# Optimization experiments

Hardware: AMD Instinct MI355X
Metric: run time of the kernel (lower is better)

## Reference

```python
import jax, jax.numpy as jnp
import numpy as np

N, E, G = 50000, 640000, 2000
F_NODE, F_EDGE, H, L, T = 64, 16, 128, 2, 2


def _seg_softmax(logits, idx, num_seg):
    # logits: [E], idx: [E] -> softmax per segment
    m = jax.ops.segment_max(logits, idx, num_segments=num_seg)
    e = jnp.exp(logits - m[idx])
    s = jax.ops.segment_sum(e, idx, num_segments=num_seg)
    return e / (s[idx] + 1e-16)


def _gru(x, h, Wih, Whh, bih, bhh):
    gi = x @ Wih + bih
    gh = h @ Whh + bhh
    ir, iz, inn = jnp.split(gi, 3, axis=-1)
    hr, hz, hn = jnp.split(gh, 3, axis=-1)
    r = jax.nn.sigmoid(ir + hr)
    z = jax.nn.sigmoid(iz + hz)
    n = jnp.tanh(inn + r * hn)
    return (1.0 - z) * n + z * h


def setup_inputs() -> dict:
    key = jax.random.key(0)
    ks = jax.random.split(key, 30)
    s = 0.05
    inp = {
        'x': jax.random.normal(ks[0], (N, F_NODE), jnp.float32),
        'edge_index': jax.random.randint(ks[1], (2, E), 0, N, jnp.int32),
        'edge_attr': jax.random.normal(ks[2], (E, F_EDGE), jnp.float32),
        'batch': jnp.sort(jax.random.randint(ks[3], (N,), 0, G, jnp.int32)),
        'emb_W': jax.random.normal(ks[4], (F_NODE, H), jnp.float32) * s,
        'emb_b': jnp.zeros((H,), jnp.float32),
        'attW1': jax.random.normal(ks[5], (L, 2 * H + F_EDGE, H), jnp.float32) * s,
        'attb1': jnp.zeros((L, H), jnp.float32),
        'attW2': jax.random.normal(ks[6], (L, H, 1), jnp.float32) * s,
        'attb2': jnp.zeros((L, 1), jnp.float32),
        'mlpW': jax.random.normal(ks[7], (L, H + F_EDGE, H), jnp.float32) * s,
        'mlpb': jnp.zeros((L, H), jnp.float32),
        'gru_Wih': jax.random.normal(ks[8], (L, H, 3 * H), jnp.float32) * s,
        'gru_Whh': jax.random.normal(ks[9], (L, H, 3 * H), jnp.float32) * s,
        'gru_bih': jnp.zeros((L, 3 * H), jnp.float32),
        'gru_bhh': jnp.zeros((L, 3 * H), jnp.float32),
        'gattW1': jax.random.normal(ks[10], (H, H), jnp.float32) * s,
        'gattb1': jnp.zeros((H,), jnp.float32),
        'gattW2': jax.random.normal(ks[11], (H, 1), jnp.float32) * s,
        'gattb2': jnp.zeros((1,), jnp.float32),
        'ggru_Wih': jax.random.normal(ks[12], (H, 3 * H), jnp.float32) * s,
        'ggru_Whh': jax.random.normal(ks[13], (H, 3 * H), jnp.float32) * s,
        'ggru_bih': jnp.zeros((3 * H,), jnp.float32),
        'ggru_bhh': jnp.zeros((3 * H,), jnp.float32),
    }
    return inp


def reference(x, edge_index, edge_attr, batch, emb_W, emb_b, attW1, attb1,
              attW2, attb2, mlpW, mlpb, gru_Wih, gru_Whh, gru_bih, gru_bhh,
              gattW1, gattb1, gattW2, gattb2, ggru_Wih, ggru_Whh, ggru_bih,
              ggru_bhh):
    src, dst = edge_index[0], edge_index[1]  # PyG: x_j = x[src], x_i = x[dst]
    h = jax.nn.relu(x @ emb_W + emb_b)  # [N, H]
    for l in range(L):
        x_i, x_j = h[dst], h[src]                       # [E, H] gathers
        cat = jnp.concatenate([x_i, x_j, edge_attr], axis=-1)  # [E, 2H+F_e]
        a = jax.nn.leaky_relu(cat @ attW1[l] + attb1[l], 0.2) @ attW2[l] + attb2[l]
        alpha = _seg_softmax(a[:, 0], dst, N)[:, None]  # segment softmax over dst
        msg = jax.nn.relu(jnp.concatenate([x_j, edge_attr], axis=-1) @ mlpW[l] + mlpb[l])
        aggr = jax.ops.segment_sum(alpha * msg, dst, num_segments=N)  # [N, H]
        h = _gru(aggr, h, gru_Wih[l], gru_Whh[l], gru_bih[l], gru_bhh[l])
    g = jax.ops.segment_sum(h, batch, num_segments=G)  # global_add_pool [G, H]
    for _ in range(T):
        s = jnp.tanh(h @ gattW1 + gattb1) @ gattW2 + gattb2  # [N, 1]
        att = _seg_softmax(s[:, 0], batch, G)[:, None]
        ctx = jax.ops.segment_sum(att * h, batch, num_segments=G)
        g = _gru(ctx, g, ggru_Wih, ggru_Whh, ggru_bih, ggru_bhh)
    return g
```

## Files before the change

### kernel.cpp

```cpp
#include <hip/hip_runtime.h>
#include <hip/hip_bf16.h>
#include <math.h>

#define N_NODES 50000
#define N_EDGES 640000
#define N_GRAPHS 2000
#define FN 64
#define FE 16
#define H 128
#define NL 2
#define DPW 4
#define SCB 1024

typedef __attribute__((ext_vector_type(8))) short short8;
typedef __attribute__((ext_vector_type(4))) float float4v;
typedef __hip_bfloat16 bf16;

static constexpr size_t AL = 256;
static constexpr size_t alup(size_t x) { return (x + AL - 1) & ~(AL - 1); }

static constexpr size_t SZ_HF    = (size_t)N_NODES * H * 4;
static constexpr size_t SZ_HB    = (size_t)N_NODES * H * 2;
static constexpr size_t SZ_XB    = (size_t)N_NODES * FN * 2;
static constexpr size_t SZ_PQMB  = (size_t)N_NODES * 384 * 2;
static constexpr size_t SZ_GH    = (size_t)N_NODES * 384 * 4;
static constexpr size_t SZ_GI    = (size_t)N_NODES * 384 * 4;
static constexpr size_t SZ_AGB   = (size_t)N_NODES * H * 2;
static constexpr size_t SZ_NF    = (size_t)N_NODES * 4;
static constexpr size_t SZ_WT    = (size_t)768 * 128 * 2;
static constexpr size_t SZ_WIHT  = (size_t)384 * 128 * 2;
static constexpr size_t SZ_EMBT  = (size_t)128 * 64 * 2;
static constexpr size_t SZ_BBIG  = (size_t)768 * 4;
static constexpr size_t SZ_G128  = (size_t)N_GRAPHS * 128 * 4;
static constexpr size_t SZ_G384  = (size_t)N_GRAPHS * 384 * 4;
static constexpr size_t SZ_GF    = (size_t)N_GRAPHS * 4;
static constexpr size_t SZ_CSE   = (size_t)N_EDGES * 8;
static constexpr size_t SZ_BSUM  = 256 * 4;

static constexpr size_t OFF_H0    = 0;
static constexpr size_t OFF_H1    = alup(OFF_H0 + SZ_HF);
static constexpr size_t OFF_H0B   = alup(OFF_H1 + SZ_HF);
static constexpr size_t OFF_H1B   = alup(OFF_H0B + SZ_HB);
static constexpr size_t OFF_XB    = alup(OFF_H1B + SZ_HB);
static constexpr size_t OFF_PQMB  = alup(OFF_XB + SZ_XB);
static constexpr size_t OFF_GH    = alup(OFF_PQMB + SZ_PQMB);
static constexpr size_t OFF_GI    = alup(OFF_GH + SZ_GH);
static constexpr size_t OFF_AGB   = alup(OFF_GI + SZ_GI);
static constexpr size_t OFF_ES    = alup(OFF_AGB + SZ_AGB);
static constexpr size_t OFF_WT    = alup(OFF_ES + SZ_NF);
static constexpr size_t OFF_WIHT  = alup(OFF_WT + SZ_WT);
static constexpr size_t OFF_EMBT  = alup(OFF_WIHT + SZ_WIHT);
static constexpr size_t OFF_BBIG  = alup(OFF_EMBT + SZ_EMBT);
static constexpr size_t OFF_G0    = alup(OFF_BBIG + SZ_BBIG);
static constexpr size_t OFF_GA    = alup(OFF_G0 + SZ_G128);
static constexpr size_t OFF_CTX   = alup(OFF_GA + SZ_G128);
static constexpr size_t OFF_GICTX = alup(OFF_CTX + SZ_G128);
static constexpr size_t OFF_GHB   = alup(OFF_GICTX + SZ_G384);
static constexpr size_t OFF_GSUM  = alup(OFF_GHB + SZ_G384);
static constexpr size_t OFF_DEG   = alup(OFF_GSUM + SZ_GF);
static constexpr size_t OFF_OFFS  = alup(OFF_DEG + SZ_NF);
static constexpr size_t OFF_CUR   = alup(OFF_OFFS + SZ_NF + 4);
static constexpr size_t OFF_CSE   = alup(OFF_CUR + SZ_NF);
static constexpr size_t OFF_GHIST = alup(OFF_CSE + SZ_CSE);
static constexpr size_t OFF_GOFFS = alup(OFF_GHIST + SZ_GF);
static constexpr size_t OFF_BSUM  = alup(OFF_GOFFS + SZ_GF + 4);
static constexpr size_t TOTAL_WS  = alup(OFF_BSUM + SZ_BSUM);

__device__ unsigned char g_afp_ws[TOTAL_WS];

__device__ inline float bf2f(unsigned short u) {
    unsigned int x = ((unsigned int)u) << 16;
    return __uint_as_float(x);
}

template<int K>
__global__ __launch_bounds__(256) void gemm_mfma(
    const bf16* __restrict__ Abf, const bf16* __restrict__ Btbf,
    const float* __restrict__ bias, float* __restrict__ C,
    bf16* __restrict__ Cb, bf16* __restrict__ Cb2,
    int M, int Ncol, int mode)
{
    const unsigned short* A  = (const unsigned short*)Abf;
    const unsigned short* Bt = (const unsigned short*)Btbf;
    const int l  = threadIdx.x & 63;
    const int w  = threadIdx.x >> 6;
    const int wm = w >> 1, wn = w & 1;
    const int row0 = blockIdx.x * 64 + wm * 32;
    const int col0 = blockIdx.y * 64 + wn * 32;
    const int lr = l & 15;
    const int lk = (l >> 4) * 8;
    float4v acc[2][2] = {};
    #pragma unroll
    for (int k0 = 0; k0 < K; k0 += 32) {
        short8 a[2], b[2];
        #pragma unroll
        for (int i = 0; i < 2; ++i) {
            int r = row0 + i * 16 + lr;
            if (r >= M) r = M - 1;
            a[i] = *(const short8*)(A + (size_t)r * K + k0 + lk);
        }
        #pragma unroll
        for (int j = 0; j < 2; ++j) {
            int c = col0 + j * 16 + lr;
            b[j] = *(const short8*)(Bt + (size_t)c * K + k0 + lk);
        }
        #pragma unroll
        for (int i = 0; i < 2; ++i)
            #pragma unroll
            for (int j = 0; j < 2; ++j)
                acc[i][j] = __builtin_amdgcn_mfma_f32_16x16x32_bf16(a[i], b[j], acc[i][j], 0, 0, 0);
    }
    const int orow = (l >> 4) * 4;
    const int ocol = l & 15;
    #pragma unroll
    for (int i = 0; i < 2; ++i) {
        #pragma unroll
        for (int j = 0; j < 2; ++j) {
            const int gc = col0 + j * 16 + ocol;
            const float bi = bias ? bias[gc] : 0.f;
            #pragma unroll
            for (int r = 0; r < 4; ++r) {
                const int gr = row0 + i * 16 + orow + r;
                if (gr >= M) continue;
                float v = acc[i][j][r] + bi;
                if (mode & 1) v = fmaxf(v, 0.f);
                if (mode & 2) {
                    if (gc < 384) Cb[(size_t)gr * 384 + gc] = __float2bfloat16(v);
                    else          Cb2[(size_t)gr * 384 + (gc - 384)] = __float2bfloat16(v);
                } else {
                    C[(size_t)gr * Ncol + gc] = v;
                    if (mode & 4) Cb[(size_t)gr * Ncol + gc] = __float2bfloat16(v);
                }
            }
        }
    }
}

__global__ __launch_bounds__(256) void gemm_gru(
    const bf16* __restrict__ Abf, const bf16* __restrict__ Btbf,
    const float* __restrict__ bias, const bf16* __restrict__ ghb,
    const float* __restrict__ hold, float* __restrict__ hnew,
    bf16* __restrict__ hnewb, int M)
{
    const unsigned short* A  = (const unsigned short*)Abf;
    const unsigned short* Bt = (const unsigned short*)Btbf;
    const unsigned short* gh = (const unsigned short*)ghb;
    const int l  = threadIdx.x & 63;
    const int w  = threadIdx.x >> 6;
    const int row0 = blockIdx.x * 64 + w * 16;
    const int lr = l & 15;
    const int lk = (l >> 4) * 8;
    float4v acc[24] = {};
    #pragma unroll
    for (int k0 = 0; k0 < 128; k0 += 32) {
        int r = row0 + lr;
        if (r >= M) r = M - 1;
        short8 a = *(const short8*)(A + (size_t)r * 128 + k0 + lk);
        #pragma unroll
        for (int j = 0; j < 24; ++j) {
            short8 b = *(const short8*)(Bt + (size_t)(j * 16 + lr) * 128 + k0 + lk);
            acc[j] = __builtin_amdgcn_mfma_f32_16x16x32_bf16(a, b, acc[j], 0, 0, 0);
        }
    }
    const int orow = (l >> 4) * 4;
    const int ocol = l & 15;
    #pragma unroll
    for (int a_ = 0; a_ < 8; ++a_) {
        const int c = a_ * 16 + ocol;
        const float bir = bias[c], biz = bias[c + 128], bin = bias[c + 256];
        #pragma unroll
        for (int r = 0; r < 4; ++r) {
            const int gr = row0 + orow + r;
            if (gr >= M) continue;
            float ir = acc[a_][r] + bir;
            float iz = acc[a_ + 8][r] + biz;
            float in = acc[a_ + 16][r] + bin;
            const unsigned short* ghp = gh + (size_t)gr * 384;
            float hr = bf2f(ghp[c]);
            float hz = bf2f(ghp[128 + c]);
            float hn = bf2f(ghp[256 + c]);
            float rg = 1.f / (1.f + __expf(-(ir + hr)));
            float zg = 1.f / (1.f + __expf(-(iz + hz)));
            float ng = tanhf(in + rg * hn);
            float hv = hold[(size_t)gr * 128 + c];
            float o = (1.f - zg) * ng + zg * hv;
            hnew[(size_t)gr * 128 + c] = o;
            hnewb[(size_t)gr * 128 + c] = __float2bfloat16(o);
        }
    }
}

#define GBM 64
#define GBN 64
#define GBK 32
__global__ __launch_bounds__(256) void gemm_f32(
    const float* __restrict__ A, const float* __restrict__ B,
    const float* __restrict__ bias, float* __restrict__ C,
    int M, int K, int Ncol)
{
    __shared__ float As[GBK][GBM + 4];
    __shared__ float Bs[GBK][GBN + 4];
    const int tx = threadIdx.x & 15;
    const int ty = threadIdx.x >> 4;
    const int row0 = blockIdx.x * GBM;
    const int col0 = blockIdx.y * GBN;
    float acc[4][4] = {};
    for (int k0 = 0; k0 < K; k0 += GBK) {
        for (int i = threadIdx.x; i < GBM * GBK; i += 256) {
            int r = i / GBK, c = i % GBK;
            float v = 0.f;
            if (row0 + r < M) v = A[(size_t)(row0 + r) * K + k0 + c];
            As[c][r] = v;
        }
        for (int i = threadIdx.x; i < GBK * GBN; i += 256) {
            int r = i / GBN, c = i % GBN;
            float v = 0.f;
            if (col0 + c < Ncol) v = B[(size_t)(k0 + r) * Ncol + col0 + c];
            Bs[r][c] = v;
        }
        __syncthreads();
        #pragma unroll
        for (int k = 0; k < GBK; ++k) {
            float a[4], b[4];
            #pragma unroll
            for (int i = 0; i < 4; ++i) a[i] = As[k][ty * 4 + i];
            #pragma unroll
            for (int j = 0; j < 4; ++j) b[j] = Bs[k][tx * 4 + j];
            #pragma unroll
            for (int i = 0; i < 4; ++i)
                #pragma unroll
                for (int j = 0; j < 4; ++j)
                    acc[i][j] = fmaf(a[i], b[j], acc[i][j]);
        }
        __syncthreads();
    }
    #pragma unroll
    for (int i = 0; i < 4; ++i) {
        int r = row0 + ty * 4 + i;
        if (r >= M) continue;
        #pragma unroll
        for (int j = 0; j < 4; ++j) {
            int c = col0 + tx * 4 + j;
            if (c >= Ncol) continue;
            C[(size_t)r * Ncol + c] = acc[i][j] + (bias ? bias[c] : 0.f);
        }
    }
}

__global__ void pack_weights_bt(const float* __restrict__ attW1,
                                const float* __restrict__ mlpW,
                                const float* __restrict__ whh,
                                const float* __restrict__ attb1,
                                const float* __restrict__ mlpb,
                                const float* __restrict__ bhh,
                                bf16* __restrict__ wt, float* __restrict__ bbig)
{
    int idx = blockIdx.x * blockDim.x + threadIdx.x;
    if (idx >= 768 * 128) return;
    int j = idx >> 7, k = idx & 127;
    float v;
    if (j < 128)      v = attW1[k * 128 + j];
    else if (j < 256) v = attW1[(128 + k) * 128 + (j - 128)];
    else if (j < 384) v = mlpW[k * 128 + (j - 256)];
    else              v = whh[k * 384 + (j - 384)];
    wt[idx] = __float2bfloat16(v);
    if (k == 0) {
        float b;
        if (j < 128)      b = attb1[j];
        else if (j < 256) b = 0.f;
        else if (j < 384) b = mlpb[j - 256];
        else              b = bhh[j - 384];
        bbig[j] = b;
    }
}

__global__ void transpose_cast(const float* __restrict__ in, bf16* __restrict__ out,
                               int K, int Ncol)
{
    int idx = blockIdx.x * blockDim.x + threadIdx.x;
    if (idx >= K * Ncol) return;
    int k = idx / Ncol, j = idx % Ncol;
    out[(size_t)j * K + k] = __float2bfloat16(in[idx]);
}

__global__ void cast_bf16_kernel(const float* __restrict__ in, bf16* __restrict__ out, int n)
{
    int idx = blockIdx.x * blockDim.x + threadIdx.x;
    if (idx < n) out[idx] = __float2bfloat16(in[idx]);
}

__global__ void hist_dst_kernel(const int* __restrict__ ei, int* __restrict__ deg) {
    int e = blockIdx.x * blockDim.x + threadIdx.x;
    if (e < N_EDGES) atomicAdd(&deg[ei[N_EDGES + e]], 1);
}
__global__ void hist_batch_kernel(const int* __restrict__ batch, int* __restrict__ hist) {
    int n = blockIdx.x * blockDim.x + threadIdx.x;
    if (n < N_NODES) atomicAdd(&hist[batch[n]], 1);
}

__global__ __launch_bounds__(1024) void scan_local(const int* __restrict__ in,
        int* __restrict__ out, int* __restrict__ bsum, int n)
{
    __shared__ int buf[SCB];
    int i = blockIdx.x * SCB + threadIdx.x;
    int v = (i < n) ? in[i] : 0;
    buf[threadIdx.x] = v;
    __syncthreads();
    #pragma unroll
    for (int off = 1; off < SCB; off <<= 1) {
        int t = (threadIdx.x >= off) ? buf[threadIdx.x - off] : 0;
        __syncthreads();
        buf[threadIdx.x] += t;
        __syncthreads();
    }
    if (i < n) out[i] = buf[threadIdx.x] - v;
    if (threadIdx.x == SCB - 1) bsum[blockIdx.x] = buf[SCB - 1];
}
__global__ __launch_bounds__(1024) void scan_bsum(int* __restrict__ bsum, int nb,
        int* __restrict__ total_dst)
{
    __shared__ int buf[SCB];
    int v = (threadIdx.x < nb) ? bsum[threadIdx.x] : 0;
    buf[threadIdx.x] = v;
    __syncthreads();
    #pragma unroll
    for (int off = 1; off < SCB; off <<= 1) {
        int t = (threadIdx.x >= off) ? buf[threadIdx.x - off] : 0;
        __syncthreads();
        buf[threadIdx.x] += t;
        __syncthreads();
    }
    if (threadIdx.x < nb) bsum[threadIdx.x] = buf[threadIdx.x] - v;
    if (threadIdx.x == 0) *total_dst = buf[SCB - 1];
}
__global__ __launch_bounds__(1024) void scan_addoff(int* __restrict__ out,
        const int* __restrict__ bsum, int n)
{
    int i = blockIdx.x * SCB + threadIdx.x;
    if (i < n) out[i] += bsum[blockIdx.x];
}

__global__ void scatter_cse_kernel(const int* __restrict__ ei, const int* __restrict__ offs,
                                   int* __restrict__ cur, int2* __restrict__ cse) {
    int e = blockIdx.x * blockDim.x + threadIdx.x;
    if (e >= N_EDGES) return;
    int d = ei[N_EDGES + e];
    int pos = offs[d] + atomicAdd(&cur[d], 1);
    cse[pos] = make_int2(ei[e], e);
}

__global__ __launch_bounds__(256, 2) void edge_fused_kernel(
    const bf16* __restrict__ pqm_b,
    const int2* __restrict__ cse, const float* __restrict__ ea,
    const float* __restrict__ w1c_g, const float* __restrict__ w2_g,
    const float* __restrict__ b2_g, const float* __restrict__ mlpw2_g,
    const int* __restrict__ offs, bf16* __restrict__ aggrb)
{
    const unsigned short* pqm = (const unsigned short*)pqm_b;
    const int wv = threadIdx.x >> 6, lane = threadIdx.x & 63;
    const int c0 = lane * 2;
    float w1r[16][2], wmr[16][2];
    #pragma unroll
    for (int k = 0; k < 16; ++k) {
        w1r[k][0] = w1c_g[k * 128 + c0];
        w1r[k][1] = w1c_g[k * 128 + c0 + 1];
        wmr[k][0] = mlpw2_g[k * 128 + c0];
        wmr[k][1] = mlpw2_g[k * 128 + c0 + 1];
    }
    const float w20 = w2_g[c0], w21 = w2_g[c0 + 1];
    const float b2 = b2_g[0];
    const int dbase = __builtin_amdgcn_readfirstlane((blockIdx.x * 4 + wv) * DPW);

    for (int rep = 0; rep < DPW; ++rep) {
        const int d = dbase + rep;
        if (d >= N_NODES) break;
        const ushort2 pu = *(const ushort2*)(pqm + (size_t)d * 384 + c0);
        const float p0 = bf2f(pu.x), p1 = bf2f(pu.y);
        float acc0 = 0.f, acc1 = 0.f, ssum = 0.f;
        const int b = offs[d], en = offs[d + 1];
        if (b < en) {
            int2 se = cse[b];
            const unsigned short* ps = pqm + (size_t)se.x * 384;
            ushort2 qu = *(const ushort2*)(ps + 128 + c0);
            ushort2 mu = *(const ushort2*)(ps + 256 + c0);
            const float4* eap = (const float4*)(ea + (size_t)se.y * 16);
            float4 e0 = eap[0], e1 = eap[1], e2 = eap[2], e3 = eap[3];
            float sp_p = 0.f, m0_p = 0.f, m1_p = 0.f, gate = 0.f;
            for (int i = b; i < en; ++i) {
                float t0 = p0 + bf2f(qu.x), t1 = p1 + bf2f(qu.y);
                float m0 = bf2f(mu.x), m1 = bf2f(mu.y);
                float er[16];
                er[0]=e0.x; er[1]=e0.y; er[2]=e0.z; er[3]=e0.w;
                er[4]=e1.x; er[5]=e1.y; er[6]=e1.z; er[7]=e1.w;
                er[8]=e2.x; er[9]=e2.y; er[10]=e2.z; er[11]=e2.w;
                er[12]=e3.x; er[13]=e3.y; er[14]=e3.z; er[15]=e3.w;
                if (i + 1 < en) {
                    se = cse[i + 1];
                    const unsigned short* psn = pqm + (size_t)se.x * 384;
                    qu = *(const ushort2*)(psn + 128 + c0);
                    mu = *(const ushort2*)(psn + 256 + c0);
                    const float4* eapn = (const float4*)(ea + (size_t)se.y * 16);
                    e0 = eapn[0]; e1 = eapn[1]; e2 = eapn[2]; e3 = eapn[3];
                }
                float sps = sp_p;
                #pragma unroll
                for (int off = 32; off; off >>= 1) sps += __shfl_xor(sps, off);
                const float ex = gate * __expf(sps + b2);
                ssum += ex;
                acc0 = fmaf(ex, fmaxf(m0_p, 0.f), acc0);
                acc1 = fmaf(ex, fmaxf(m1_p, 0.f), acc1);
                #pragma unroll
                for (int k = 0; k < 16; ++k) {
                    t0 = fmaf(er[k], w1r[k][0], t0);
                    t1 = fmaf(er[k], w1r[k][1], t1);
                    m0 = fmaf(er[k], wmr[k][0], m0);
                    m1 = fmaf(er[k], wmr[k][1], m1);
                }
                float a0 = (t0 > 0.f) ? t0 : 0.2f * t0;
                float a1 = (t1 > 0.f) ? t1 : 0.2f * t1;
                sp_p = a0 * w20 + a1 * w21;
                m0_p = m0; m1_p = m1;
                gate = 1.f;
            }
            float sps = sp_p;
            #pragma unroll
            for (int off = 32; off; off >>= 1) sps += __shfl_xor(sps, off);
            const float ex = __expf(sps + b2);
            ssum += ex;
            acc0 = fmaf(ex, fmaxf(m0_p, 0.f), acc0);
            acc1 = fmaf(ex, fmaxf(m1_p, 0.f), acc1);
        }
        const float inv = 1.f / (ssum + 1e-16f);
        bf16* outp = aggrb + (size_t)d * 128 + c0;
        outp[0] = __float2bfloat16(acc0 * inv);
        outp[1] = __float2bfloat16(acc1 * inv);
    }
}

__global__ void gru_elem_kernel(const float* __restrict__ gi,
                                const float* __restrict__ gh,
                                const float* __restrict__ hold, float* __restrict__ hnew,
                                int rows)
{
    int idx = blockIdx.x * blockDim.x + threadIdx.x;
    if (idx >= rows * H) return;
    int r = idx >> 7, c = idx & 127;
    float ir = gi[(size_t)r * 384 + c];
    float iz = gi[(size_t)r * 384 + 128 + c];
    float in = gi[(size_t)r * 384 + 256 + c];
    float hr = gh[(size_t)r * 384 + c];
    float hz = gh[(size_t)r * 384 + 128 + c];
    float hn = gh[(size_t)r * 384 + 256 + c];
    float rg = 1.f / (1.f + __expf(-(ir + hr)));
    float zg = 1.f / (1.f + __expf(-(iz + hz)));
    float ng = tanhf(in + rg * hn);
    float hv = hold[idx];
    hnew[idx] = (1.f - zg) * ng + zg * hv;
}

__global__ __launch_bounds__(128) void graph_pool_sum(
    const float* __restrict__ h, const int* __restrict__ goffs, float* __restrict__ g0)
{
    int g = blockIdx.x, c = threadIdx.x;
    int b = goffs[g], e2 = goffs[g + 1];
    float acc = 0.f;
    for (int i = b; i < e2; ++i) acc += h[(size_t)i * 128 + c];
    g0[(size_t)g * 128 + c] = acc;
}

__global__ __launch_bounds__(256) void node_score2_kernel(
    const float* __restrict__ hW1, const float* __restrict__ W2,
    const float* __restrict__ b2, const int* __restrict__ batch,
    float* __restrict__ es, float* __restrict__ gsum)
{
    const int wv = threadIdx.x >> 6, lane = threadIdx.x & 63;
    const int n = blockIdx.x * 4 + wv;
    if (n >= N_NODES) return;
    const int c0 = lane * 2;
    float sp = tanhf(hW1[(size_t)n * 128 + c0]) * W2[c0]
             + tanhf(hW1[(size_t)n * 128 + c0 + 1]) * W2[c0 + 1];
    #pragma unroll
    for (int off = 32; off; off >>= 1) sp += __shfl_xor(sp, off);
    if (lane == 0) {
        float ex = __expf(sp + b2[0]);
        es[n] = ex;
        atomicAdd(&gsum[batch[n]], ex);
    }
}

__global__ __launch_bounds__(128) void graph_ctx_kernel(
    const float* __restrict__ h, const int* __restrict__ goffs,
    const float* __restrict__ es, const float* __restrict__ gsum,
    float* __restrict__ ctx)
{
    int g = blockIdx.x, c = threadIdx.x;
    float invs = 1.f / (gsum[g] + 1e-16f);
    int b = goffs[g], e2 = goffs[g + 1];
    float acc = 0.f;
    for (int i = b; i < e2; ++i) acc = fmaf(es[i] * invs, h[(size_t)i * 128 + c], acc);
    ctx[(size_t)g * 128 + c] = acc;
}

extern "C" void kernel_launch(void* const* d_in, const int* in_sizes, int n_in,
                              void* d_out, int out_size, void* d_ws, size_t ws_size,
                              hipStream_t stream) {
    const float* x      = (const float*)d_in[0];
    const int*   ei     = (const int*)d_in[1];
    const float* ea     = (const float*)d_in[2];
    const int*   batch  = (const int*)d_in[3];
    const float* embW   = (const float*)d_in[4];
    const float* embB   = (const float*)d_in[5];
    const float* attW1  = (const float*)d_in[6];
    const float* attb1  = (const float*)d_in[7];
    const float* attW2  = (const float*)d_in[8];
    const float* attb2  = (const float*)d_in[9];
    const float* mlpW   = (const float*)d_in[10];
    const float* mlpb   = (const float*)d_in[11];
    const float* gWih   = (const float*)d_in[12];
    const float* gWhh   = (const float*)d_in[13];
    const float* gbih   = (const float*)d_in[14];
    const float* gbhh   = (const float*)d_in[15];
    const float* gattW1 = (const float*)d_in[16];
    const float* gattb1 = (const float*)d_in[17];
    const float* gattW2 = (const float*)d_in[18];
    const float* gattb2 = (const float*)d_in[19];
    const float* ggWih  = (const float*)d_in[20];
    const float* ggWhh  = (const float*)d_in[21];
    const float* ggbih  = (const float*)d_in[22];
    const float* ggbhh  = (const float*)d_in[23];
    float* out = (float*)d_out;

    void* basep = nullptr;
    (void)hipGetSymbolAddress(&basep, HIP_SYMBOL(g_afp_ws));
    char* base = (char*)basep;
    float* h0    = (float*)(base + OFF_H0);
    float* h1    = (float*)(base + OFF_H1);
    bf16*  h0b   = (bf16*)(base + OFF_H0B);
    bf16*  h1b   = (bf16*)(base + OFF_H1B);
    bf16*  xb    = (bf16*)(base + OFF_XB);
    bf16*  pqmb  = (bf16*)(base + OFF_PQMB);
    bf16*  ghx   = (bf16*)(base + OFF_GH);
    float* hW1   = (float*)(base + OFF_GI);
    bf16*  aggrb = (bf16*)(base + OFF_AGB);
    float* es    = (float*)(base + OFF_ES);
    bf16*  wt    = (bf16*)(base + OFF_WT);
    bf16*  wiht  = (bf16*)(base + OFF_WIHT);
    bf16*  embt  = (bf16*)(base + OFF_EMBT);
    float* bbig  = (float*)(base + OFF_BBIG);
    float* g0b   = (float*)(base + OFF_G0);
    float* gAb   = (float*)(base + OFF_GA);
    float* ctx   = (float*)(base + OFF_CTX);
    float* gictx = (float*)(base + OFF_GICTX);
    float* ghr   = (float*)(base + OFF_GHB);
    float* gsum  = (float*)(base + OFF_GSUM);
    int*   deg   = (int*)(base + OFF_DEG);
    int*   offs  = (int*)(base + OFF_OFFS);
    int*   cur   = (int*)(base + OFF_CUR);
    int2*  cse   = (int2*)(base + OFF_CSE);
    int*   ghist = (int*)(base + OFF_GHIST);
    int*   goffs = (int*)(base + OFF_GOFFS);
    int*   bsum  = (int*)(base + OFF_BSUM);

    (void)hipMemsetAsync(deg, 0, SZ_NF, stream);
    (void)hipMemsetAsync(cur, 0, SZ_NF, stream);
    (void)hipMemsetAsync(ghist, 0, SZ_GF, stream);
    (void)hipMemsetAsync(gsum, 0, SZ_GF, stream);

    const int nbN = (N_NODES + SCB - 1) / SCB;
    const int nbG = (N_GRAPHS + SCB - 1) / SCB;

    hist_dst_kernel<<<(N_EDGES + 255) / 256, 256, 0, stream>>>(ei, deg);
    scan_local<<<nbN, SCB, 0, stream>>>(deg, offs, bsum, N_NODES);
    scan_bsum<<<1, SCB, 0, stream>>>(bsum, nbN, offs + N_NODES);
    scan_addoff<<<nbN, SCB, 0, stream>>>(offs, bsum, N_NODES);
    scatter_cse_kernel<<<(N_EDGES + 255) / 256, 256, 0, stream>>>(ei, offs, cur, cse);
    hist_batch_kernel<<<(N_NODES + 255) / 256, 256, 0, stream>>>(batch, ghist);
    scan_local<<<nbG, SCB, 0, stream>>>(ghist, goffs, bsum, N_GRAPHS);
    scan_bsum<<<1, SCB, 0, stream>>>(bsum, nbG, goffs + N_GRAPHS);
    scan_addoff<<<nbG, SCB, 0, stream>>>(goffs, bsum, N_GRAPHS);

    cast_bf16_kernel<<<(N_NODES * FN + 255) / 256, 256, 0, stream>>>(x, xb, N_NODES * FN);
    transpose_cast<<<(FN * 128 + 255) / 256, 256, 0, stream>>>(embW, embt, FN, 128);

    {
        dim3 g((N_NODES + 63) / 64, 128 / 64);
        gemm_mfma<64><<<g, 256, 0, stream>>>(xb, embt, embB, h0, h0b, nullptr,
                                             N_NODES, 128, 1 | 4);
    }

    float* hcur = h0;  bf16* hcurb = h0b;
    float* hnext = h1; bf16* hnextb = h1b;
    for (int l = 0; l < NL; ++l) {
        pack_weights_bt<<<(768 * 128 + 255) / 256, 256, 0, stream>>>(
            attW1 + (size_t)l * 272 * 128, mlpW + (size_t)l * 144 * 128,
            gWhh + (size_t)l * 128 * 384, attb1 + l * 128, mlpb + l * 128,
            gbhh + l * 384, wt, bbig);
        {
            dim3 g((N_NODES + 63) / 64, 768 / 64);
            gemm_mfma<128><<<g, 256, 0, stream>>>(hcurb, wt, bbig, nullptr, pqmb, ghx,
                                                  N_NODES, 768, 2);
        }
        edge_fused_kernel<<<(N_NODES + 4 * DPW - 1) / (4 * DPW), 256, 0, stream>>>(
            pqmb, cse, ea, attW1 + (size_t)l * 272 * 128 + 256 * 128,
            attW2 + (size_t)l * 128, attb2 + l,
            mlpW + (size_t)l * 144 * 128 + 128 * 128,
            offs, aggrb);
        transpose_cast<<<(128 * 384 + 255) / 256, 256, 0, stream>>>(
            gWih + (size_t)l * 128 * 384, wiht, 128, 384);
        gemm_gru<<<(N_NODES + 63) / 64, 256, 0, stream>>>(
            aggrb, wiht, gbih + l * 384, ghx, hcur, hnext, hnextb, N_NODES);
        float* t = hcur; hcur = hnext; hnext = t;
        bf16* tb = hcurb; hcurb = hnextb; hnextb = tb;
    }

    graph_pool_sum<<<N_GRAPHS, 128, 0, stream>>>(hcur, goffs, g0b);
    transpose_cast<<<(128 * 128 + 255) / 256, 256, 0, stream>>>(gattW1, wiht, 128, 128);
    {
        dim3 g((N_NODES + 63) / 64, 128 / 64);
        gemm_mfma<128><<<g, 256, 0, stream>>>(hcurb, wiht, gattb1, hW1, nullptr, nullptr,
                                              N_NODES, 128, 0);
    }
    node_score2_kernel<<<(N_NODES + 3) / 4, 256, 0, stream>>>(
        hW1, gattW2, gattb2, batch, es, gsum);
    graph_ctx_kernel<<<N_GRAPHS, 128, 0, stream>>>(hcur, goffs, es, gsum, ctx);

    dim3 gg((N_GRAPHS + 63) / 64, 384 / 64);
    gemm_f32<<<gg, 256, 0, stream>>>(ctx, ggWih, ggbih, gictx, N_GRAPHS, H, 384);
    gemm_f32<<<gg, 256, 0, stream>>>(g0b, ggWhh, ggbhh, ghr, N_GRAPHS, H, 384);
    gru_elem_kernel<<<((size_t)N_GRAPHS * H + 255) / 256, 256, 0, stream>>>(
        gictx, ghr, g0b, gAb, N_GRAPHS);
    gemm_f32<<<gg, 256, 0, stream>>>(gAb, ggWhh, ggbhh, ghr, N_GRAPHS, H, 384);
    gru_elem_kernel<<<((size_t)N_GRAPHS * H + 255) / 256, 256, 0, stream>>>(
        gictx, ghr, gAb, out, N_GRAPHS);
}
```

Baseline: 936.9 us.

## Keep node hidden state only in bf16 and simplify edge kernel to one node per wave

Removes the fp32 copy of the node hidden state. The GRU, pooling and context kernels now read and write only bf16 h, which cuts memory traffic and the extra stores. Separately, the edge kernel drops the 4-nodes-per-wave loop and its software-pipelined softmax reduction in favour of a simpler one-destination-per-wave loop. The bf16 recurrence lowers precision of the hidden state across layers, and the edge loop loses its overlap of the shuffle reduction with the next edge's compute.

After: 916.3 us. 1.02x faster.

```diff
diff --git a/kernel.cpp b/kernel.cpp
--- a/kernel.cpp
+++ b/kernel.cpp
@@ -9,7 +9,6 @@
 #define FE 16
 #define H 128
 #define NL 2
-#define DPW 4
 #define SCB 1024
 
 typedef __attribute__((ext_vector_type(8))) short short8;
@@ -127,6 +126,8 @@
                 if (mode & 2) {
                     if (gc < 384) Cb[(size_t)gr * 384 + gc] = __float2bfloat16(v);
                     else          Cb2[(size_t)gr * 384 + (gc - 384)] = __float2bfloat16(v);
+                } else if (mode & 8) {
+                    Cb[(size_t)gr * Ncol + gc] = __float2bfloat16(v);
                 } else {
                     C[(size_t)gr * Ncol + gc] = v;
                     if (mode & 4) Cb[(size_t)gr * Ncol + gc] = __float2bfloat16(v);
@@ -139,12 +140,12 @@
 __global__ __launch_bounds__(256) void gemm_gru(
     const bf16* __restrict__ Abf, const bf16* __restrict__ Btbf,
     const float* __restrict__ bias, const bf16* __restrict__ ghb,
-    const float* __restrict__ hold, float* __restrict__ hnew,
-    bf16* __restrict__ hnewb, int M)
+    const bf16* __restrict__ holdb, bf16* __restrict__ hnewb, int M)
 {
     const unsigned short* A  = (const unsigned short*)Abf;
     const unsigned short* Bt = (const unsigned short*)Btbf;
     const unsigned short* gh = (const unsigned short*)ghb;
+    const unsigned short* hold = (const unsigned short*)holdb;
     const int l  = threadIdx.x & 63;
     const int w  = threadIdx.x >> 6;
     const int row0 = blockIdx.x * 64 + w * 16;
@@ -182,9 +183,8 @@
             float rg = 1.f / (1.f + __expf(-(ir + hr)));
             float zg = 1.f / (1.f + __expf(-(iz + hz)));
             float ng = tanhf(in + rg * hn);
-            float hv = hold[(size_t)gr * 128 + c];
+            float hv = bf2f(hold[(size_t)gr * 128 + c]);
             float o = (1.f - zg) * ng + zg * hv;
-            hnew[(size_t)gr * 128 + c] = o;
             hnewb[(size_t)gr * 128 + c] = __float2bfloat16(o);
         }
     }
@@ -369,72 +369,58 @@
     }
     const float w20 = w2_g[c0], w21 = w2_g[c0 + 1];
     const float b2 = b2_g[0];
-    const int dbase = __builtin_amdgcn_readfirstlane((blockIdx.x * 4 + wv) * DPW);
-
-    for (int rep = 0; rep < DPW; ++rep) {
-        const int d = dbase + rep;
-        if (d >= N_NODES) break;
-        const ushort2 pu = *(const ushort2*)(pqm + (size_t)d * 384 + c0);
-        const float p0 = bf2f(pu.x), p1 = bf2f(pu.y);
-        float acc0 = 0.f, acc1 = 0.f, ssum = 0.f;
-        const int b = offs[d], en = offs[d + 1];
-        if (b < en) {
-            int2 se = cse[b];
-            const unsigned short* ps = pqm + (size_t)se.x * 384;
-            ushort2 qu = *(const ushort2*)(ps + 128 + c0);
-            ushort2 mu = *(const ushort2*)(ps + 256 + c0);
-            const float4* eap = (const float4*)(ea + (size_t)se.y * 16);
-            float4 e0 = eap[0], e1 = eap[1], e2 = eap[2], e3 = eap[3];
-            float sp_p = 0.f, m0_p = 0.f, m1_p = 0.f, gate = 0.f;
-            for (int i = b; i < en; ++i) {
-                float t0 = p0 + bf2f(qu.x), t1 = p1 + bf2f(qu.y);
-                float m0 = bf2f(mu.x), m1 = bf2f(mu.y);
-                float er[16];
-                er[0]=e0.x; er[1]=e0.y; er[2]=e0.z; er[3]=e0.w;
-                er[4]=e1.x; er[5]=e1.y; er[6]=e1.z; er[7]=e1.w;
-                er[8]=e2.x; er[9]=e2.y; er[10]=e2.z; er[11]=e2.w;
-                er[12]=e3.x; er[13]=e3.y; er[14]=e3.z; er[15]=e3.w;
-                if (i + 1 < en) {
-                    se = cse[i + 1];
-                    const unsigned short* psn = pqm + (size_t)se.x * 384;
-                    qu = *(const ushort2*)(psn + 128 + c0);
-                    mu = *(const ushort2*)(psn + 256 + c0);
-                    const float4* eapn = (const float4*)(ea + (size_t)se.y * 16);
-                    e0 = eapn[0]; e1 = eapn[1]; e2 = eapn[2]; e3 = eapn[3];
-                }
-                float sps = sp_p;
-                #pragma unroll
-                for (int off = 32; off; off >>= 1) sps += __shfl_xor(sps, off);
-                const float ex = gate * __expf(sps + b2);
-                ssum += ex;
-                acc0 = fmaf(ex, fmaxf(m0_p, 0.f), acc0);
-                acc1 = fmaf(ex, fmaxf(m1_p, 0.f), acc1);
-                #pragma unroll
-                for (int k = 0; k < 16; ++k) {
-                    t0 = fmaf(er[k], w1r[k][0], t0);
-                    t1 = fmaf(er[k], w1r[k][1], t1);
-                    m0 = fmaf(er[k], wmr[k][0], m0);
-                    m1 = fmaf(er[k], wmr[k][1], m1);
-                }
-                float a0 = (t0 > 0.f) ? t0 : 0.2f * t0;
-                float a1 = (t1 > 0.f) ? t1 : 0.2f * t1;
-                sp_p = a0 * w20 + a1 * w21;
-                m0_p = m0; m1_p = m1;
-                gate = 1.f;
+    const int d = __builtin_amdgcn_readfirstlane(blockIdx.x * 4 + wv);
+    if (d >= N_NODES) return;
+
+    const ushort2 pu = *(const ushort2*)(pqm + (size_t)d * 384 + c0);
+    const float p0 = bf2f(pu.x), p1 = bf2f(pu.y);
+    float acc0 = 0.f, acc1 = 0.f, ssum = 0.f;
+    const int b = offs[d], en = offs[d + 1];
+    if (b < en) {
+        int2 se = cse[b];
+        const unsigned short* ps = pqm + (size_t)se.x * 384;
+        ushort2 qu = *(const ushort2*)(ps + 128 + c0);
+        ushort2 mu = *(const ushort2*)(ps + 256 + c0);
+        const float4* eap = (const float4*)(ea + (size_t)se.y * 16);
+        float4 e0 = eap[0], e1 = eap[1], e2 = eap[2], e3 = eap[3];
+        for (int i = b; i < en; ++i) {
+            float t0 = p0 + bf2f(qu.x), t1 = p1 + bf2f(qu.y);
+            float m0 = bf2f(mu.x), m1 = bf2f(mu.y);
+            float er[16];
+            er[0]=e0.x; er[1]=e0.y; er[2]=e0.z; er[3]=e0.w;
+            er[4]=e1.x; er[5]=e1.y; er[6]=e1.z; er[7]=e1.w;
+            er[8]=e2.x; er[9]=e2.y; er[10]=e2.z; er[11]=e2.w;
+            er[12]=e3.x; er[13]=e3.y; er[14]=e3.z; er[15]=e3.w;
+            if (i + 1 < en) {
+                se = cse[i + 1];
+                const unsigned short* psn = pqm + (size_t)se.x * 384;
+                qu = *(const ushort2*)(psn + 128 + c0);
+                mu = *(const ushort2*)(psn + 256 + c0);
+                const float4* eapn = (const float4*)(ea + (size_t)se.y * 16);
+                e0 = eapn[0]; e1 = eapn[1]; e2 = eapn[2]; e3 = eapn[3];
             }
-            float sps = sp_p;
             #pragma unroll
-            for (int off = 32; off; off >>= 1) sps += __shfl_xor(sps, off);
-            const float ex = __expf(sps + b2);
+            for (int k = 0; k < 16; ++k) {
+                t0 = fmaf(er[k], w1r[k][0], t0);
+                t1 = fmaf(er[k], w1r[k][1], t1);
+                m0 = fmaf(er[k], wmr[k][0], m0);
+                m1 = fmaf(er[k], wmr[k][1], m1);
+            }
+            float a0 = (t0 > 0.f) ? t0 : 0.2f * t0;
+            float a1 = (t1 > 0.f) ? t1 : 0.2f * t1;
+            float sp = a0 * w20 + a1 * w21;
+            #pragma unroll
+            for (int off = 32; off; off >>= 1) sp += __shfl_xor(sp, off);
+            const float ex = __expf(sp + b2);
             ssum += ex;
-            acc0 = fmaf(ex, fmaxf(m0_p, 0.f), acc0);
-            acc1 = fmaf(ex, fmaxf(m1_p, 0.f), acc1);
-        }
-        const float inv = 1.f / (ssum + 1e-16f);
-        bf16* outp = aggrb + (size_t)d * 128 + c0;
-        outp[0] = __float2bfloat16(acc0 * inv);
-        outp[1] = __float2bfloat16(acc1 * inv);
-    }
+            acc0 = fmaf(ex, fmaxf(m0, 0.f), acc0);
+            acc1 = fmaf(ex, fmaxf(m1, 0.f), acc1);
+        }
+    }
+    const float inv = 1.f / (ssum + 1e-16f);
+    bf16* outp = aggrb + (size_t)d * 128 + c0;
+    outp[0] = __float2bfloat16(acc0 * inv);
+    outp[1] = __float2bfloat16(acc1 * inv);
 }
 
 __global__ void gru_elem_kernel(const float* __restrict__ gi,
@@ -459,12 +445,13 @@
 }
 
 __global__ __launch_bounds__(128) void graph_pool_sum(
-    const float* __restrict__ h, const int* __restrict__ goffs, float* __restrict__ g0)
-{
+    const bf16* __restrict__ hb, const int* __restrict__ goffs, float* __restrict__ g0)
+{
+    const unsigned short* h = (const unsigned short*)hb;
     int g = blockIdx.x, c = threadIdx.x;
     int b = goffs[g], e2 = goffs[g + 1];
     float acc = 0.f;
-    for (int i = b; i < e2; ++i) acc += h[(size_t)i * 128 + c];
+    for (int i = b; i < e2; ++i) acc += bf2f(h[(size_t)i * 128 + c]);
     g0[(size_t)g * 128 + c] = acc;
 }
 
@@ -489,15 +476,16 @@
 }
 
 __global__ __launch_bounds__(128) void graph_ctx_kernel(
-    const float* __restrict__ h, const int* __restrict__ goffs,
+    const bf16* __restrict__ hb, const int* __restrict__ goffs,
     const float* __restrict__ es, const float* __restrict__ gsum,
     float* __restrict__ ctx)
 {
+    const unsigned short* h = (const unsigned short*)hb;
     int g = blockIdx.x, c = threadIdx.x;
     float invs = 1.f / (gsum[g] + 1e-16f);
     int b = goffs[g], e2 = goffs[g + 1];
     float acc = 0.f;
-    for (int i = b; i < e2; ++i) acc = fmaf(es[i] * invs, h[(size_t)i * 128 + c], acc);
+    for (int i = b; i < e2; ++i) acc = fmaf(es[i] * invs, bf2f(h[(size_t)i * 128 + c]), acc);
     ctx[(size_t)g * 128 + c] = acc;
 }
 
@@ -533,8 +521,6 @@
     void* basep = nullptr;
     (void)hipGetSymbolAddress(&basep, HIP_SYMBOL(g_afp_ws));
     char* base = (char*)basep;
-    float* h0    = (float*)(base + OFF_H0);
-    float* h1    = (float*)(base + OFF_H1);
     bf16*  h0b   = (bf16*)(base + OFF_H0B);
     bf16*  h1b   = (bf16*)(base + OFF_H1B);
     bf16*  xb    = (bf16*)(base + OFF_XB);
@@ -584,12 +570,12 @@
 
     {
         dim3 g((N_NODES + 63) / 64, 128 / 64);
-        gemm_mfma<64><<<g, 256, 0, stream>>>(xb, embt, embB, h0, h0b, nullptr,
-                                             N_NODES, 128, 1 | 4);
-    }
-
-    float* hcur = h0;  bf16* hcurb = h0b;
-    float* hnext = h1; bf16* hnextb = h1b;
+        gemm_mfma<64><<<g, 256, 0, stream>>>(xb, embt, embB, nullptr, h0b, nullptr,
+                                             N_NODES, 128, 1 | 8);
+    }
+
+    bf16* hcurb = h0b;
+    bf16* hnextb = h1b;
     for (int l = 0; l < NL; ++l) {
         pack_weights_bt<<<(768 * 128 + 255) / 256, 256, 0, stream>>>(
             attW1 + (size_t)l * 272 * 128, mlpW + (size_t)l * 144 * 128,
@@ -600,7 +586,7 @@
             gemm_mfma<128><<<g, 256, 0, stream>>>(hcurb, wt, bbig, nullptr, pqmb, ghx,
                                                   N_NODES, 768, 2);
         }
-        edge_fused_kernel<<<(N_NODES + 4 * DPW - 1) / (4 * DPW), 256, 0, stream>>>(
+        edge_fused_kernel<<<(N_NODES + 3) / 4, 256, 0, stream>>>(
             pqmb, cse, ea, attW1 + (size_t)l * 272 * 128 + 256 * 128,
             attW2 + (size_t)l * 128, attb2 + l,
             mlpW + (size_t)l * 144 * 128 + 128 * 128,
@@ -608,12 +594,11 @@
         transpose_cast<<<(128 * 384 + 255) / 256, 256, 0, stream>>>(
             gWih + (size_t)l * 128 * 384, wiht, 128, 384);
         gemm_gru<<<(N_NODES + 63) / 64, 256, 0, stream>>>(
-            aggrb, wiht, gbih + l * 384, ghx, hcur, hnext, hnextb, N_NODES);
-        float* t = hcur; hcur = hnext; hnext = t;
+            aggrb, wiht, gbih + l * 384, ghx, hcurb, hnextb, N_NODES);
         bf16* tb = hcurb; hcurb = hnextb; hnextb = tb;
     }
 
-    graph_pool_sum<<<N_GRAPHS, 128, 0, stream>>>(hcur, goffs, g0b);
+    graph_pool_sum<<<N_GRAPHS, 128, 0, stream>>>(hcurb, goffs, g0b);
     transpose_cast<<<(128 * 128 + 255) / 256, 256, 0, stream>>>(gattW1, wiht, 128, 128);
     {
         dim3 g((N_NODES + 63) / 64, 128 / 64);
@@ -622,7 +607,7 @@
     }
     node_score2_kernel<<<(N_NODES + 3) / 4, 256, 0, stream>>>(
         hW1, gattW2, gattb2, batch, es, gsum);
-    graph_ctx_kernel<<<N_GRAPHS, 128, 0, stream>>>(hcur, goffs, es, gsum, ctx);
+    graph_ctx_kernel<<<N_GRAPHS, 128, 0, stream>>>(hcurb, goffs, es, gsum, ctx);
 
     dim3 gg((N_GRAPHS + 63) / 64, 384 / 64);
     gemm_f32<<<gg, 256, 0, stream>>>(ctx, ggWih, ggbih, gictx, N_GRAPHS, H, 384);
```
